# Performance work log

Measured on AMD Instinct MI355X. Metric: run time of the kernel, lower is better.

## Reference

```python
import jax, jax.numpy as jnp
import numpy as np

B, N, D = 4, 2048, 768
OUT = 768

def setup_inputs() -> dict:
    key = jax.random.key(0)
    k1, k2 = jax.random.split(key)
    x = jax.random.normal(k1, (B, N, D), dtype=jnp.float32)
    kernel = jax.random.normal(k2, (3, D, OUT), dtype=jnp.float32) * 0.02
    return {"x": x, "kernel": kernel}

def reference(x, kernel):
    # Single-head attention with shared QKV kernel stack [3, D, OUT]
    q = jnp.einsum('bnd,do->bno', x, kernel[0])
    k = jnp.einsum('bnd,do->bno', x, kernel[1])
    v = jnp.einsum('bnd,do->bno', x, kernel[2])
    # NOTE: original divides by 64**0.5 == 8 regardless of dims (faithful)
    scores = jnp.einsum('bqo,bko->bqk', q, k) / 8.0
    attn = jax.nn.softmax(scores, axis=-1)
    return jnp.einsum('bqk,bko->bqo', attn, v)
```

## Files before the change

### kernel.cpp

```cpp
#include <hip/hip_runtime.h>
#include <hip/hip_bf16.h>

constexpr int B_ = 4, N_ = 2048, D_ = 768, OUT_ = 768;
constexpr int M_ = B_ * N_;

typedef __attribute__((ext_vector_type(8))) short short8;
typedef __attribute__((ext_vector_type(4))) float floatx4;

__device__ __forceinline__ unsigned short f2bfu(float f) {
    union { __hip_bfloat16 b; unsigned short u; } cv;
    cv.b = __float2bfloat16(f);
    return cv.u;
}

#define GLOAD_LDS16(g, l)                                                     \
    __builtin_amdgcn_global_load_lds(                                         \
        (const __attribute__((address_space(1))) void*)(g),                   \
        (__attribute__((address_space(3))) void*)(l), 16, 0, 0)

template <int BM>
__device__ __forceinline__ void gemm_core(
    const __hip_bfloat16* __restrict__ a_base, int lda,
    const __hip_bfloat16* __restrict__ b_base, int ldb,
    int m0, int n0, int K,
    __hip_bfloat16* As, __hip_bfloat16* Bs,
    floatx4 (&acc)[BM / 32][4]) {
    constexpr int MF = BM / 32;
    const int tid  = threadIdx.x;
    const int wave = tid >> 6, lane = tid & 63;
    const int wm = (wave >> 1) * (BM / 2), wn = (wave & 1) * 64;
    const int lrow = lane & 15, kq = lane >> 4;
    const int sw = lrow & 7;

    for (int k0 = 0; k0 < K; k0 += 64) {
#pragma unroll
        for (int i = 0; i < MF; ++i) {
            const int u = i * 256 + tid;
            const int row = u >> 3, cg = (u & 7) ^ (row & 7);
            const __hip_bfloat16* g =
                a_base + (size_t)(m0 + row) * lda + k0 + cg * 8;
            GLOAD_LDS16(g, As + (size_t)(i * 256 + wave * 64) * 8);
        }
#pragma unroll
        for (int i = 0; i < 4; ++i) {
            const int u = i * 256 + tid;
            const int row = u >> 3, cg = (u & 7) ^ (row & 7);
            const __hip_bfloat16* g =
                b_base + (size_t)(n0 + row) * ldb + k0 + cg * 8;
            GLOAD_LDS16(g, Bs + (size_t)(i * 256 + wave * 64) * 8);
        }
        __syncthreads();

#pragma unroll
        for (int s = 0; s < 2; ++s) {
            short8 af[MF], bfr[4];
#pragma unroll
            for (int t = 0; t < MF; ++t) {
                const int row = wm + t * 16 + lrow;
                const int slot = (s * 4 + kq) ^ sw;
                af[t] = *(const short8*)(As + row * 64 + slot * 8);
            }
#pragma unroll
            for (int t = 0; t < 4; ++t) {
                const int row = wn + t * 16 + lrow;
                const int slot = (s * 4 + kq) ^ sw;
                bfr[t] = *(const short8*)(Bs + row * 64 + slot * 8);
            }
#pragma unroll
            for (int mi = 0; mi < MF; ++mi)
#pragma unroll
                for (int ni = 0; ni < 4; ++ni)
                    acc[mi][ni] = __builtin_amdgcn_mfma_f32_16x16x32_bf16(
                        af[mi], bfr[ni], acc[mi][ni], 0, 0, 0);
        }
        __syncthreads();
    }
}

__global__ __launch_bounds__(256)
void prep(const float* __restrict__ x, const float* __restrict__ w,
          __hip_bfloat16* __restrict__ xb, __hip_bfloat16* __restrict__ wt,
          float* __restrict__ l) {
    __shared__ float t[32][33];
    const int tid = threadIdx.x;
    if (blockIdx.x < 3072) {
        const size_t i = (size_t)blockIdx.x * 2048 + (size_t)tid * 8;
        float4 a = *(const float4*)(x + i);
        float4 b = *(const float4*)(x + i + 4);
        *(ushort4*)((unsigned short*)xb + i) =
            make_ushort4(f2bfu(a.x), f2bfu(a.y), f2bfu(a.z), f2bfu(a.w));
        *(ushort4*)((unsigned short*)xb + i + 4) =
            make_ushort4(f2bfu(b.x), f2bfu(b.y), f2bfu(b.z), f2bfu(b.w));
    } else if (blockIdx.x < 4800) {
        const int bid = blockIdx.x - 3072;
        const int s = bid / 576, rem = bid % 576;
        const int d0 = (rem / 24) * 32, o0 = (rem % 24) * 32;
        const int tx = tid & 31, ty = tid >> 5;
        const float* ws = w + (size_t)s * D_ * OUT_;
        __hip_bfloat16* wts = wt + (size_t)s * OUT_ * D_;
#pragma unroll
        for (int i = 0; i < 4; ++i)
            t[ty + 8 * i][tx] = ws[(size_t)(d0 + ty + 8 * i) * OUT_ + o0 + tx];
        __syncthreads();
#pragma unroll
        for (int i = 0; i < 4; ++i)
            wts[(size_t)(o0 + ty + 8 * i) * D_ + d0 + tx] =
                __float2bfloat16(t[tx][ty + 8 * i]);
    } else {
        float4* l4 = (float4*)l;
#pragma unroll
        for (int i = 0; i < 8; ++i) l4[i * 256 + tid] = make_float4(0, 0, 0, 0);
    }
}

__global__ __launch_bounds__(256)
void qkv_mfma(const __hip_bfloat16* __restrict__ xb,
              const __hip_bfloat16* __restrict__ wt,
              __hip_bfloat16* __restrict__ q, __hip_bfloat16* __restrict__ k,
              __hip_bfloat16* __restrict__ vt) {
    __shared__ __align__(16) char smem[34816];
    __hip_bfloat16* As = (__hip_bfloat16*)smem;
    __hip_bfloat16* Bs = As + 128 * 64;
    const int s = blockIdx.z;
    const int m0 = blockIdx.x * 128, n0 = blockIdx.y * 128;
    floatx4 acc[4][4] = {};
    gemm_core<128>(xb, D_, wt + (size_t)s * OUT_ * D_, D_, m0, n0, D_, As, Bs,
                   acc);

    const int tid = threadIdx.x, wave = tid >> 6, lane = tid & 63;
    const int wm = (wave >> 1) * 64, wn = (wave & 1) * 64;
    const int lrow = lane & 15, kq = lane >> 4;
    unsigned short* E = (unsigned short*)smem;

    if (s < 2) {
#pragma unroll
        for (int mi = 0; mi < 4; ++mi)
#pragma unroll
            for (int ni = 0; ni < 4; ++ni) {
                const int n = wn + ni * 16 + lrow;
#pragma unroll
                for (int r = 0; r < 4; ++r)
                    E[(wm + mi * 16 + kq * 4 + r) * 136 + n] =
                        f2bfu(acc[mi][ni][r]);
            }
    } else {
#pragma unroll
        for (int mi = 0; mi < 4; ++mi)
#pragma unroll
            for (int ni = 0; ni < 4; ++ni) {
                const int n = wn + ni * 16 + lrow;
#pragma unroll
                for (int r = 0; r < 4; ++r)
                    E[n * 136 + wm + mi * 16 + kq * 4 + r] =
                        f2bfu(acc[mi][ni][r]);
            }
    }
    __syncthreads();

    if (s < 2) {
        __hip_bfloat16* out = (s == 0) ? q : k;
#pragma unroll
        for (int i = 0; i < 8; ++i) {
            const int u = i * 256 + tid, row = u >> 4, c = u & 15;
            short8 v = *(const short8*)(E + row * 136 + c * 8);
            *(short8*)(out + (size_t)(m0 + row) * OUT_ + n0 + c * 8) = v;
        }
    } else {
        const int b = m0 >> 11, j0 = m0 & 2047;
#pragma unroll
        for (int i = 0; i < 8; ++i) {
            const int u = i * 256 + tid, nrow = u >> 4, c = u & 15;
            short8 v = *(const short8*)(E + nrow * 136 + c * 8);
            *(short8*)(vt + ((size_t)b * OUT_ + n0 + nrow) * N_ + j0 + c * 8) =
                v;
        }
    }
}

__global__ __launch_bounds__(256)
void scores_mfma(const __hip_bfloat16* __restrict__ q,
                 const __hip_bfloat16* __restrict__ k,
                 __hip_bfloat16* __restrict__ pt, float* __restrict__ l) {
    __shared__ __align__(16) char smem[34816];
    __hip_bfloat16* As = (__hip_bfloat16*)smem;
    __hip_bfloat16* Bs = As + 128 * 64;
    const int b = blockIdx.z;
    const int m0 = blockIdx.x * 128, n0 = blockIdx.y * 128;
    floatx4 acc[4][4] = {};
    gemm_core<128>(q + (size_t)b * N_ * OUT_, OUT_,
                   k + (size_t)b * N_ * OUT_, OUT_, m0, n0, OUT_, As, Bs, acc);

    const int tid = threadIdx.x, wave = tid >> 6, lane = tid & 63;
    const int wm = (wave >> 1) * 64, wn = (wave & 1) * 64;
    const int lrow = lane & 15, kq = lane >> 4;

    float rs[4][4];
#pragma unroll
    for (int mi = 0; mi < 4; ++mi)
#pragma unroll
        for (int r = 0; r < 4; ++r) rs[mi][r] = 0.0f;
#pragma unroll
    for (int mi = 0; mi < 4; ++mi)
#pragma unroll
        for (int ni = 0; ni < 4; ++ni)
#pragma unroll
            for (int r = 0; r < 4; ++r) {
                const float e = __expf(acc[mi][ni][r] * 0.125f - 8.0f);
                acc[mi][ni][r] = e;
                rs[mi][r] += e;
            }
#pragma unroll
    for (int mi = 0; mi < 4; ++mi)
#pragma unroll
        for (int r = 0; r < 4; ++r) {
            float v = rs[mi][r];
            v += __shfl_xor(v, 1, 64);
            v += __shfl_xor(v, 2, 64);
            v += __shfl_xor(v, 4, 64);
            v += __shfl_xor(v, 8, 64);
            if (lrow == 0)
                atomicAdd(&l[(size_t)b * N_ + m0 + wm + mi * 16 + kq * 4 + r],
                          v);
        }

    unsigned short* E = (unsigned short*)smem;
#pragma unroll
    for (int mi = 0; mi < 4; ++mi)
#pragma unroll
        for (int ni = 0; ni < 4; ++ni) {
            const int n = wn + ni * 16 + lrow;
#pragma unroll
            for (int r = 0; r < 4; ++r)
                E[(wm + mi * 16 + kq * 4 + r) * 136 + n] =
                    f2bfu(acc[mi][ni][r]);
        }
    __syncthreads();
    __hip_bfloat16* pb = pt + (size_t)b * N_ * N_;
#pragma unroll
    for (int i = 0; i < 8; ++i) {
        const int u = i * 256 + tid, row = u >> 4, c = u & 15;
        short8 v = *(const short8*)(E + row * 136 + c * 8);
        *(short8*)(pb + (size_t)(m0 + row) * N_ + n0 + c * 8) = v;
    }
}

__global__ __launch_bounds__(256)
void pv_mfma(const __hip_bfloat16* __restrict__ pt,
             const __hip_bfloat16* __restrict__ vt,
             const float* __restrict__ l, float* __restrict__ out) {
    __shared__ __align__(16) __hip_bfloat16 As[64 * 64];
    __shared__ __align__(16) __hip_bfloat16 Bs[128 * 64];
    const int b = blockIdx.z;
    const int m0 = blockIdx.x * 64, n0 = blockIdx.y * 128;
    floatx4 acc[2][4] = {};
    gemm_core<64>(pt + (size_t)b * N_ * N_, N_,
                  vt + (size_t)b * OUT_ * N_, N_, m0, n0, N_, As, Bs, acc);

    const int tid = threadIdx.x, wave = tid >> 6, lane = tid & 63;
    const int wm = (wave >> 1) * 32, wn = (wave & 1) * 64;
    const int lrow = lane & 15, kq = lane >> 4;
    const float* lb = l + (size_t)b * N_;
    float inv[2][4];
#pragma unroll
    for (int mi = 0; mi < 2; ++mi)
#pragma unroll
        for (int r = 0; r < 4; ++r)
            inv[mi][r] = 1.0f / lb[m0 + wm + mi * 16 + kq * 4 + r];
#pragma unroll
    for (int mi = 0; mi < 2; ++mi)
#pragma unroll
        for (int ni = 0; ni < 4; ++ni) {
            const int n = n0 + wn + ni * 16 + lrow;
#pragma unroll
            for (int r = 0; r < 4; ++r) {
                const int i = m0 + wm + mi * 16 + kq * 4 + r;
                out[((size_t)b * N_ + i) * OUT_ + n] =
                    acc[mi][ni][r] * inv[mi][r];
            }
        }
}

extern "C" void kernel_launch(void* const* d_in, const int* in_sizes, int n_in,
                              void* d_out, int out_size, void* d_ws, size_t ws_size,
                              hipStream_t stream) {
    const float* x = (const float*)d_in[0];
    const float* w = (const float*)d_in[1];
    float* out = (float*)d_out;

    __hip_bfloat16* q  = (__hip_bfloat16*)d_ws;
    __hip_bfloat16* k  = q + (size_t)M_ * OUT_;
    __hip_bfloat16* vt = k + (size_t)M_ * OUT_;
    __hip_bfloat16* xb = vt + (size_t)M_ * OUT_;
    __hip_bfloat16* wt = xb + (size_t)M_ * D_;
    float* l = (float*)(wt + (size_t)3 * OUT_ * D_);
    __hip_bfloat16* pt = (__hip_bfloat16*)(l + M_);

    prep<<<dim3(4801), dim3(256), 0, stream>>>(x, w, xb, wt, l);
    qkv_mfma<<<dim3(M_ / 128, OUT_ / 128, 3), dim3(256), 0, stream>>>(
        xb, wt, q, k, vt);
    scores_mfma<<<dim3(N_ / 128, N_ / 128, B_), dim3(256), 0, stream>>>(
        q, k, pt, l);
    pv_mfma<<<dim3(N_ / 64, OUT_ / 128, B_), dim3(256), 0, stream>>>(
        pt, vt, l, out);
}
```

Baseline: 202.2 us.

## Use 256x256 tiles with 4-stage async LDS pipeline and split-K PV

Replaces the 128x128 (and 64x128) GEMM core with a 512-thread 256x256 tile core that uses a 4-deep ring of direct global-to-LDS loads, explicit vmcnt waits and MFMA priority boosting. Epilogues for q, k and scores now store directly from registers without LDS staging. PV is split into two K halves that accumulate into a zero-initialized output with float atomics, which is why prep now also clears the output. The aim is more operand reuse per tile and overlap of loads with MFMA work. In exchange it uses 128 KB of LDS, makes fewer and larger blocks that may underfill the GPU, and adds atomic traffic.

After: 227.5 us. 1.13x slower.

```diff
diff --git a/kernel.cpp b/kernel.cpp
--- a/kernel.cpp
+++ b/kernel.cpp
@@ -18,69 +18,95 @@
         (const __attribute__((address_space(1))) void*)(g),                   \
         (__attribute__((address_space(3))) void*)(l), 16, 0, 0)
 
-template <int BM>
-__device__ __forceinline__ void gemm_core(
-    const __hip_bfloat16* __restrict__ a_base, int lda,
-    const __hip_bfloat16* __restrict__ b_base, int ldb,
-    int m0, int n0, int K,
-    __hip_bfloat16* As, __hip_bfloat16* Bs,
-    floatx4 (&acc)[BM / 32][4]) {
-    constexpr int MF = BM / 32;
-    const int tid  = threadIdx.x;
+template <int NT>
+__device__ __forceinline__ void gemm256_core(
+    const __hip_bfloat16* __restrict__ aG, int lda,
+    const __hip_bfloat16* __restrict__ bG, int ldb,
+    unsigned short* LDS, floatx4 (&acc)[8][4]) {
+    const int tid = threadIdx.x;
     const int wave = tid >> 6, lane = tid & 63;
-    const int wm = (wave >> 1) * (BM / 2), wn = (wave & 1) * 64;
     const int lrow = lane & 15, kq = lane >> 4;
-    const int sw = lrow & 7;
-
-    for (int k0 = 0; k0 < K; k0 += 64) {
-#pragma unroll
-        for (int i = 0; i < MF; ++i) {
-            const int u = i * 256 + tid;
-            const int row = u >> 3, cg = (u & 7) ^ (row & 7);
-            const __hip_bfloat16* g =
-                a_base + (size_t)(m0 + row) * lda + k0 + cg * 8;
-            GLOAD_LDS16(g, As + (size_t)(i * 256 + wave * 64) * 8);
-        }
-#pragma unroll
-        for (int i = 0; i < 4; ++i) {
-            const int u = i * 256 + tid;
-            const int row = u >> 3, cg = (u & 7) ^ (row & 7);
-            const __hip_bfloat16* g =
-                b_base + (size_t)(n0 + row) * ldb + k0 + cg * 8;
-            GLOAD_LDS16(g, Bs + (size_t)(i * 256 + wave * 64) * 8);
-        }
-        __syncthreads();
-
-#pragma unroll
-        for (int s = 0; s < 2; ++s) {
-            short8 af[MF], bfr[4];
-#pragma unroll
-            for (int t = 0; t < MF; ++t) {
-                const int row = wm + t * 16 + lrow;
-                const int slot = (s * 4 + kq) ^ sw;
-                af[t] = *(const short8*)(As + row * 64 + slot * 8);
-            }
-#pragma unroll
-            for (int t = 0; t < 4; ++t) {
-                const int row = wn + t * 16 + lrow;
-                const int slot = (s * 4 + kq) ^ sw;
-                bfr[t] = *(const short8*)(Bs + row * 64 + slot * 8);
-            }
-#pragma unroll
-            for (int mi = 0; mi < MF; ++mi)
-#pragma unroll
-                for (int ni = 0; ni < 4; ++ni)
-                    acc[mi][ni] = __builtin_amdgcn_mfma_f32_16x16x32_bf16(
-                        af[mi], bfr[ni], acc[mi][ni], 0, 0, 0);
-        }
-        __syncthreads();
-    }
+    const int wm = (wave >> 2) * 128, wn = (wave & 3) * 64;
+
+    const __hip_bfloat16* sA[2];
+    const __hip_bfloat16* sB[2];
+#pragma unroll
+    for (int i = 0; i < 2; ++i) {
+        const int u = i * 512 + tid;
+        const int p = u >> 3, g = (u & 7) ^ (p & 7);
+        const int row = 2 * p + (g >> 2), ch = g & 3;
+        sA[i] = aG + (size_t)row * lda + ch * 8;
+        sB[i] = bG + (size_t)row * ldb + ch * 8;
+    }
+    int offA[8], offB[4];
+#pragma unroll
+    for (int mi = 0; mi < 8; ++mi) {
+        const int row = wm + mi * 16 + lrow;
+        const int p = row >> 1, g = ((row & 1) << 2) | kq;
+        offA[mi] = p * 64 + ((g ^ (p & 7)) * 8);
+    }
+#pragma unroll
+    for (int ni = 0; ni < 4; ++ni) {
+        const int row = wn + ni * 16 + lrow;
+        const int p = row >> 1, g = ((row & 1) << 2) | kq;
+        offB[ni] = p * 64 + ((g ^ (p & 7)) * 8);
+    }
+
+#define STAGE_T(ti)                                                        \
+    do {                                                                   \
+        unsigned short* dst_ = LDS + ((ti) & 3) * 16384 + wave * 512;      \
+        GLOAD_LDS16(sA[0], dst_);                                          \
+        GLOAD_LDS16(sA[1], dst_ + 4096);                                   \
+        GLOAD_LDS16(sB[0], dst_ + 8192);                                   \
+        GLOAD_LDS16(sB[1], dst_ + 12288);                                  \
+        sA[0] += 32; sA[1] += 32; sB[0] += 32; sB[1] += 32;                \
+    } while (0)
+
+    STAGE_T(0);
+    STAGE_T(1);
+    STAGE_T(2);
+    asm volatile("s_waitcnt vmcnt(8)" ::: "memory");
+    __builtin_amdgcn_s_barrier();
+    __builtin_amdgcn_sched_barrier(0);
+
+    for (int t = 0; t < NT; ++t) {
+        if (t + 3 < NT) STAGE_T(t + 3);
+        const unsigned short* Sa = LDS + (t & 3) * 16384;
+        const unsigned short* Sb = Sa + 8192;
+        short8 bf[4], af[8];
+#pragma unroll
+        for (int ni = 0; ni < 4; ++ni)
+            bf[ni] = *(const short8*)(Sb + offB[ni]);
+#pragma unroll
+        for (int mi = 0; mi < 8; ++mi)
+            af[mi] = *(const short8*)(Sa + offA[mi]);
+        __builtin_amdgcn_s_setprio(1);
+#pragma unroll
+        for (int mi = 0; mi < 8; ++mi)
+#pragma unroll
+            for (int ni = 0; ni < 4; ++ni)
+                acc[mi][ni] = __builtin_amdgcn_mfma_f32_16x16x32_bf16(
+                    af[mi], bf[ni], acc[mi][ni], 0, 0, 0);
+        __builtin_amdgcn_s_setprio(0);
+        if (t + 3 < NT) {
+            asm volatile("s_waitcnt vmcnt(8)" ::: "memory");
+        } else if (t + 2 < NT) {
+            asm volatile("s_waitcnt vmcnt(4)" ::: "memory");
+        } else if (t + 1 < NT) {
+            asm volatile("s_waitcnt vmcnt(0)" ::: "memory");
+        }
+        if (t + 1 < NT) {
+            __builtin_amdgcn_s_barrier();
+            __builtin_amdgcn_sched_barrier(0);
+        }
+    }
+#undef STAGE_T
 }
 
 __global__ __launch_bounds__(256)
 void prep(const float* __restrict__ x, const float* __restrict__ w,
           __hip_bfloat16* __restrict__ xb, __hip_bfloat16* __restrict__ wt,
-          float* __restrict__ l) {
+          float* __restrict__ l, float* __restrict__ out) {
     __shared__ float t[32][33];
     const int tid = threadIdx.x;
     if (blockIdx.x < 3072) {
@@ -106,101 +132,97 @@
         for (int i = 0; i < 4; ++i)
             wts[(size_t)(o0 + ty + 8 * i) * D_ + d0 + tx] =
                 __float2bfloat16(t[tx][ty + 8 * i]);
+    } else if (blockIdx.x == 4800) {
+        float4* l4 = (float4*)l;
+#pragma unroll
+        for (int i = 0; i < 8; ++i) l4[i * 256 + tid] = make_float4(0, 0, 0, 0);
     } else {
-        float4* l4 = (float4*)l;
-#pragma unroll
-        for (int i = 0; i < 8; ++i) l4[i * 256 + tid] = make_float4(0, 0, 0, 0);
-    }
-}
-
-__global__ __launch_bounds__(256)
+        const size_t bid2 = blockIdx.x - 4801;
+        ((float4*)out)[bid2 * 256 + tid] = make_float4(0, 0, 0, 0);
+    }
+}
+
+__global__ __launch_bounds__(512, 2)
 void qkv_mfma(const __hip_bfloat16* __restrict__ xb,
               const __hip_bfloat16* __restrict__ wt,
               __hip_bfloat16* __restrict__ q, __hip_bfloat16* __restrict__ k,
               __hip_bfloat16* __restrict__ vt) {
-    __shared__ __align__(16) char smem[34816];
-    __hip_bfloat16* As = (__hip_bfloat16*)smem;
-    __hip_bfloat16* Bs = As + 128 * 64;
+    __shared__ __align__(16) unsigned short LDS[65536];
     const int s = blockIdx.z;
-    const int m0 = blockIdx.x * 128, n0 = blockIdx.y * 128;
-    floatx4 acc[4][4] = {};
-    gemm_core<128>(xb, D_, wt + (size_t)s * OUT_ * D_, D_, m0, n0, D_, As, Bs,
-                   acc);
+    const int m0 = blockIdx.x * 256, n0 = blockIdx.y * 256;
+    floatx4 acc[8][4] = {};
+    gemm256_core<24>(xb + (size_t)m0 * D_, D_,
+                     wt + (size_t)s * OUT_ * D_ + (size_t)n0 * D_, D_, LDS,
+                     acc);
 
     const int tid = threadIdx.x, wave = tid >> 6, lane = tid & 63;
-    const int wm = (wave >> 1) * 64, wn = (wave & 1) * 64;
     const int lrow = lane & 15, kq = lane >> 4;
-    unsigned short* E = (unsigned short*)smem;
+    const int wm = (wave >> 2) * 128, wn = (wave & 3) * 64;
 
     if (s < 2) {
-#pragma unroll
-        for (int mi = 0; mi < 4; ++mi)
-#pragma unroll
-            for (int ni = 0; ni < 4; ++ni) {
-                const int n = wn + ni * 16 + lrow;
-#pragma unroll
-                for (int r = 0; r < 4; ++r)
-                    E[(wm + mi * 16 + kq * 4 + r) * 136 + n] =
-                        f2bfu(acc[mi][ni][r]);
+        unsigned short* outp = (unsigned short*)(s == 0 ? q : k);
+#pragma unroll
+        for (int mi = 0; mi < 8; ++mi)
+#pragma unroll
+            for (int r = 0; r < 4; ++r) {
+                const size_t ro =
+                    (size_t)(m0 + wm + mi * 16 + kq * 4 + r) * OUT_ + n0 + wn;
+#pragma unroll
+                for (int ni = 0; ni < 4; ++ni)
+                    outp[ro + ni * 16 + lrow] = f2bfu(acc[mi][ni][r]);
             }
     } else {
-#pragma unroll
-        for (int mi = 0; mi < 4; ++mi)
-#pragma unroll
-            for (int ni = 0; ni < 4; ++ni) {
-                const int n = wn + ni * 16 + lrow;
-#pragma unroll
-                for (int r = 0; r < 4; ++r)
-                    E[n * 136 + wm + mi * 16 + kq * 4 + r] =
-                        f2bfu(acc[mi][ni][r]);
+        unsigned short* E = LDS;
+        const int b = m0 >> 11, j0 = m0 & 2047;
+#pragma unroll
+        for (int h = 0; h < 2; ++h) {
+            __syncthreads();
+            if ((wave >> 2) == h) {
+#pragma unroll
+                for (int ni = 0; ni < 4; ++ni)
+#pragma unroll
+                    for (int mi = 0; mi < 8; ++mi)
+#pragma unroll
+                        for (int r = 0; r < 4; ++r)
+                            E[(wn + ni * 16 + lrow) * 136 + mi * 16 + kq * 4 +
+                              r] = f2bfu(acc[mi][ni][r]);
             }
-    }
-    __syncthreads();
-
-    if (s < 2) {
-        __hip_bfloat16* out = (s == 0) ? q : k;
-#pragma unroll
-        for (int i = 0; i < 8; ++i) {
-            const int u = i * 256 + tid, row = u >> 4, c = u & 15;
-            short8 v = *(const short8*)(E + row * 136 + c * 8);
-            *(short8*)(out + (size_t)(m0 + row) * OUT_ + n0 + c * 8) = v;
-        }
-    } else {
-        const int b = m0 >> 11, j0 = m0 & 2047;
-#pragma unroll
-        for (int i = 0; i < 8; ++i) {
-            const int u = i * 256 + tid, nrow = u >> 4, c = u & 15;
-            short8 v = *(const short8*)(E + nrow * 136 + c * 8);
-            *(short8*)(vt + ((size_t)b * OUT_ + n0 + nrow) * N_ + j0 + c * 8) =
-                v;
-        }
-    }
-}
-
-__global__ __launch_bounds__(256)
+            __syncthreads();
+#pragma unroll
+            for (int i = 0; i < 8; ++i) {
+                const int u = i * 512 + tid, nr = u >> 4, c = u & 15;
+                short8 vv = *(const short8*)(E + nr * 136 + c * 8);
+                *(short8*)((unsigned short*)vt +
+                           ((size_t)b * OUT_ + n0 + nr) * N_ + j0 + h * 128 +
+                           c * 8) = vv;
+            }
+        }
+    }
+}
+
+__global__ __launch_bounds__(512, 2)
 void scores_mfma(const __hip_bfloat16* __restrict__ q,
                  const __hip_bfloat16* __restrict__ k,
                  __hip_bfloat16* __restrict__ pt, float* __restrict__ l) {
-    __shared__ __align__(16) char smem[34816];
-    __hip_bfloat16* As = (__hip_bfloat16*)smem;
-    __hip_bfloat16* Bs = As + 128 * 64;
+    __shared__ __align__(16) unsigned short LDS[65536];
     const int b = blockIdx.z;
-    const int m0 = blockIdx.x * 128, n0 = blockIdx.y * 128;
-    floatx4 acc[4][4] = {};
-    gemm_core<128>(q + (size_t)b * N_ * OUT_, OUT_,
-                   k + (size_t)b * N_ * OUT_, OUT_, m0, n0, OUT_, As, Bs, acc);
+    const int m0 = blockIdx.x * 256, n0 = blockIdx.y * 256;
+    floatx4 acc[8][4] = {};
+    gemm256_core<24>(q + (size_t)b * N_ * OUT_ + (size_t)m0 * OUT_, OUT_,
+                     k + (size_t)b * N_ * OUT_ + (size_t)n0 * OUT_, OUT_, LDS,
+                     acc);
 
     const int tid = threadIdx.x, wave = tid >> 6, lane = tid & 63;
-    const int wm = (wave >> 1) * 64, wn = (wave & 1) * 64;
     const int lrow = lane & 15, kq = lane >> 4;
-
-    float rs[4][4];
-#pragma unroll
-    for (int mi = 0; mi < 4; ++mi)
+    const int wm = (wave >> 2) * 128, wn = (wave & 3) * 64;
+
+    float rs[8][4];
+#pragma unroll
+    for (int mi = 0; mi < 8; ++mi)
 #pragma unroll
         for (int r = 0; r < 4; ++r) rs[mi][r] = 0.0f;
 #pragma unroll
-    for (int mi = 0; mi < 4; ++mi)
+    for (int mi = 0; mi < 8; ++mi)
 #pragma unroll
         for (int ni = 0; ni < 4; ++ni)
 #pragma unroll
@@ -210,7 +232,7 @@
                 rs[mi][r] += e;
             }
 #pragma unroll
-    for (int mi = 0; mi < 4; ++mi)
+    for (int mi = 0; mi < 8; ++mi)
 #pragma unroll
         for (int r = 0; r < 4; ++r) {
             float v = rs[mi][r];
@@ -222,67 +244,53 @@
                 atomicAdd(&l[(size_t)b * N_ + m0 + wm + mi * 16 + kq * 4 + r],
                           v);
         }
-
-    unsigned short* E = (unsigned short*)smem;
-#pragma unroll
-    for (int mi = 0; mi < 4; ++mi)
-#pragma unroll
-        for (int ni = 0; ni < 4; ++ni) {
-            const int n = wn + ni * 16 + lrow;
-#pragma unroll
-            for (int r = 0; r < 4; ++r)
-                E[(wm + mi * 16 + kq * 4 + r) * 136 + n] =
-                    f2bfu(acc[mi][ni][r]);
-        }
-    __syncthreads();
-    __hip_bfloat16* pb = pt + (size_t)b * N_ * N_;
-#pragma unroll
-    for (int i = 0; i < 8; ++i) {
-        const int u = i * 256 + tid, row = u >> 4, c = u & 15;
-        short8 v = *(const short8*)(E + row * 136 + c * 8);
-        *(short8*)(pb + (size_t)(m0 + row) * N_ + n0 + c * 8) = v;
-    }
-}
-
-__global__ __launch_bounds__(256)
+    unsigned short* pb = (unsigned short*)pt + (size_t)b * N_ * N_;
+#pragma unroll
+    for (int mi = 0; mi < 8; ++mi)
+#pragma unroll
+        for (int r = 0; r < 4; ++r) {
+            const size_t ro =
+                (size_t)(m0 + wm + mi * 16 + kq * 4 + r) * N_ + n0 + wn;
+#pragma unroll
+            for (int ni = 0; ni < 4; ++ni)
+                pb[ro + ni * 16 + lrow] = f2bfu(acc[mi][ni][r]);
+        }
+}
+
+__global__ __launch_bounds__(512, 2)
 void pv_mfma(const __hip_bfloat16* __restrict__ pt,
              const __hip_bfloat16* __restrict__ vt,
              const float* __restrict__ l, float* __restrict__ out) {
-    __shared__ __align__(16) __hip_bfloat16 As[64 * 64];
-    __shared__ __align__(16) __hip_bfloat16 Bs[128 * 64];
-    const int b = blockIdx.z;
-    const int m0 = blockIdx.x * 64, n0 = blockIdx.y * 128;
-    floatx4 acc[2][4] = {};
-    gemm_core<64>(pt + (size_t)b * N_ * N_, N_,
-                  vt + (size_t)b * OUT_ * N_, N_, m0, n0, N_, As, Bs, acc);
+    __shared__ __align__(16) unsigned short LDS[65536];
+    const int b = blockIdx.z >> 1, h = blockIdx.z & 1;
+    const int m0 = blockIdx.x * 256, n0 = blockIdx.y * 256;
+    floatx4 acc[8][4] = {};
+    gemm256_core<32>(
+        pt + (size_t)b * N_ * N_ + (size_t)m0 * N_ + h * 1024, N_,
+        vt + (size_t)b * OUT_ * N_ + (size_t)n0 * N_ + h * 1024, N_, LDS, acc);
 
     const int tid = threadIdx.x, wave = tid >> 6, lane = tid & 63;
-    const int wm = (wave >> 1) * 32, wn = (wave & 1) * 64;
     const int lrow = lane & 15, kq = lane >> 4;
-    const float* lb = l + (size_t)b * N_;
-    float inv[2][4];
-#pragma unroll
-    for (int mi = 0; mi < 2; ++mi)
-#pragma unroll
-        for (int r = 0; r < 4; ++r)
-            inv[mi][r] = 1.0f / lb[m0 + wm + mi * 16 + kq * 4 + r];
-#pragma unroll
-    for (int mi = 0; mi < 2; ++mi)
-#pragma unroll
-        for (int ni = 0; ni < 4; ++ni) {
-            const int n = n0 + wn + ni * 16 + lrow;
-#pragma unroll
-            for (int r = 0; r < 4; ++r) {
-                const int i = m0 + wm + mi * 16 + kq * 4 + r;
-                out[((size_t)b * N_ + i) * OUT_ + n] =
-                    acc[mi][ni][r] * inv[mi][r];
-            }
+    const int wm = (wave >> 2) * 128, wn = (wave & 3) * 64;
+    const float* lb = l + (size_t)b * N_ + m0 + wm;
+#pragma unroll
+    for (int mi = 0; mi < 8; ++mi)
+#pragma unroll
+        for (int r = 0; r < 4; ++r) {
+            const float inv = 1.0f / lb[mi * 16 + kq * 4 + r];
+            float* o = out +
+                       ((size_t)b * N_ + m0 + wm + mi * 16 + kq * 4 + r) *
+                           OUT_ +
+                       n0 + wn;
+#pragma unroll
+            for (int ni = 0; ni < 4; ++ni)
+                atomicAdd(o + ni * 16 + lrow, acc[mi][ni][r] * inv);
         }
 }
 
 extern "C" void kernel_launch(void* const* d_in, const int* in_sizes, int n_in,
-                              void* d_out, int out_size, void* d_ws, size_t ws_size,
-                              hipStream_t stream) {
+                              void* d_out, int out_size, void* d_ws,
+                              size_t ws_size, hipStream_t stream) {
     const float* x = (const float*)d_in[0];
     const float* w = (const float*)d_in[1];
     float* out = (float*)d_out;
@@ -295,11 +303,8 @@
     float* l = (float*)(wt + (size_t)3 * OUT_ * D_);
     __hip_bfloat16* pt = (__hip_bfloat16*)(l + M_);
 
-    prep<<<dim3(4801), dim3(256), 0, stream>>>(x, w, xb, wt, l);
-    qkv_mfma<<<dim3(M_ / 128, OUT_ / 128, 3), dim3(256), 0, stream>>>(
-        xb, wt, q, k, vt);
-    scores_mfma<<<dim3(N_ / 128, N_ / 128, B_), dim3(256), 0, stream>>>(
-        q, k, pt, l);
-    pv_mfma<<<dim3(N_ / 64, OUT_ / 128, B_), dim3(256), 0, stream>>>(
-        pt, vt, l, out);
-}
+    prep<<<dim3(10945), dim3(256), 0, stream>>>(x, w, xb, wt, l, out);
+    qkv_mfma<<<dim3(32, 3, 3), dim3(512), 0, stream>>>(xb, wt, q, k, vt);
+    scores_mfma<<<dim3(8, 8, 4), dim3(512), 0, stream>>>(q, k, pt, l);
+    pv_mfma<<<dim3(8, 3, 8), dim3(512), 0, stream>>>(pt, vt, l, out);
+}
```

## Triple-buffer GEMM mainloop with async LDS loads and larger 512-thread tiles

Applied to the files above, without the earlier changes.

Replaces the single-buffered K-loop GEMM core with a three-stage ring buffer fed by direct global-to-LDS loads. It issues the loads two K-steps ahead and synchronises with explicit vmcnt waits and one barrier per step, so memory traffic overlaps MFMA work. The K step drops from 64 to 32, and the LDS layout pairs rows with an XOR swizzle. Blocks grow to 512 threads with larger output tiles (128x256 for QKV and scores, 128x128 for PV), trading fewer blocks and lower occupancy for more operand reuse. The epilogues are adjusted to the new tile shapes, and the PV output store is reordered per row.

New measurement: 189.7 us. 1.07x faster.

```diff
diff --git a/kernel.cpp b/kernel.cpp
--- a/kernel.cpp
+++ b/kernel.cpp
@@ -18,62 +18,89 @@
         (const __attribute__((address_space(1))) void*)(g),                   \
         (__attribute__((address_space(3))) void*)(l), 16, 0, 0)
 
-template <int BM>
-__device__ __forceinline__ void gemm_core(
-    const __hip_bfloat16* __restrict__ a_base, int lda,
-    const __hip_bfloat16* __restrict__ b_base, int ldb,
-    int m0, int n0, int K,
-    __hip_bfloat16* As, __hip_bfloat16* Bs,
-    floatx4 (&acc)[BM / 32][4]) {
-    constexpr int MF = BM / 32;
-    const int tid  = threadIdx.x;
+#define MFMA_BF16 __builtin_amdgcn_mfma_f32_16x16x32_bf16
+#define SBAR __builtin_amdgcn_s_barrier
+#define SCHED0 __builtin_amdgcn_sched_barrier
+
+template <int MFR, int NT>
+__device__ __forceinline__ void gemm_tb(
+    const __hip_bfloat16* __restrict__ aG, int lda,
+    const __hip_bfloat16* __restrict__ bG, int ldb,
+    unsigned short* LDS, floatx4 (&acc)[MFR][4]) {
+    constexpr int BSLOT = (MFR == 4) ? 8192 : 4096;
+    constexpr int BUFS = 4096 + BSLOT;
+    constexpr int LOADS = (MFR == 4) ? 3 : 2;
+    const int tid = threadIdx.x;
     const int wave = tid >> 6, lane = tid & 63;
-    const int wm = (wave >> 1) * (BM / 2), wn = (wave & 1) * 64;
-    const int lrow = lane & 15, kq = lane >> 4;
-    const int sw = lrow & 7;
-
-    for (int k0 = 0; k0 < K; k0 += 64) {
-#pragma unroll
-        for (int i = 0; i < MF; ++i) {
-            const int u = i * 256 + tid;
-            const int row = u >> 3, cg = (u & 7) ^ (row & 7);
-            const __hip_bfloat16* g =
-                a_base + (size_t)(m0 + row) * lda + k0 + cg * 8;
-            GLOAD_LDS16(g, As + (size_t)(i * 256 + wave * 64) * 8);
-        }
-#pragma unroll
-        for (int i = 0; i < 4; ++i) {
-            const int u = i * 256 + tid;
-            const int row = u >> 3, cg = (u & 7) ^ (row & 7);
-            const __hip_bfloat16* g =
-                b_base + (size_t)(n0 + row) * ldb + k0 + cg * 8;
-            GLOAD_LDS16(g, Bs + (size_t)(i * 256 + wave * 64) * 8);
-        }
-        __syncthreads();
-
-#pragma unroll
-        for (int s = 0; s < 2; ++s) {
-            short8 af[MF], bfr[4];
-#pragma unroll
-            for (int t = 0; t < MF; ++t) {
-                const int row = wm + t * 16 + lrow;
-                const int slot = (s * 4 + kq) ^ sw;
-                af[t] = *(const short8*)(As + row * 64 + slot * 8);
-            }
-#pragma unroll
-            for (int t = 0; t < 4; ++t) {
-                const int row = wn + t * 16 + lrow;
-                const int slot = (s * 4 + kq) ^ sw;
-                bfr[t] = *(const short8*)(Bs + row * 64 + slot * 8);
-            }
-#pragma unroll
-            for (int mi = 0; mi < MF; ++mi)
-#pragma unroll
-                for (int ni = 0; ni < 4; ++ni)
-                    acc[mi][ni] = __builtin_amdgcn_mfma_f32_16x16x32_bf16(
-                        af[mi], bfr[ni], acc[mi][ni], 0, 0, 0);
-        }
-        __syncthreads();
+    const int lr = lane & 15, kq = lane >> 4;
+    const int wm = (MFR == 4) ? (wave >> 2) * 64 : (wave >> 1) * 32;
+    const int wn = (MFR == 4) ? (wave & 3) * 64 : (wave & 1) * 64;
+
+    const int p0 = tid >> 3, g0 = (tid & 7) ^ (p0 & 7);
+    const __hip_bfloat16* pa =
+        aG + (size_t)(2 * p0 + (g0 >> 2)) * lda + (g0 & 3) * 8;
+    const __hip_bfloat16* pb0 =
+        bG + (size_t)(2 * p0 + (g0 >> 2)) * ldb + (g0 & 3) * 8;
+    const __hip_bfloat16* pb1 = bG;
+    if constexpr (MFR == 4) {
+        const int u = 512 + tid, p1 = u >> 3, g1 = (u & 7) ^ (p1 & 7);
+        pb1 = bG + (size_t)(2 * p1 + (g1 >> 2)) * ldb + (g1 & 3) * 8;
+    }
+
+    int oa[MFR], ob[4];
+#pragma unroll
+    for (int mi = 0; mi < MFR; ++mi) {
+        const int r = wm + mi * 16 + lr, p = r >> 1;
+        const int g = ((r & 1) << 2) | kq;
+        oa[mi] = p * 64 + ((g ^ (p & 7)) * 8);
+    }
+#pragma unroll
+    for (int ni = 0; ni < 4; ++ni) {
+        const int r = wn + ni * 16 + lr, p = r >> 1;
+        const int g = ((r & 1) << 2) | kq;
+        ob[ni] = p * 64 + ((g ^ (p & 7)) * 8);
+    }
+
+    auto STAGE = [&](int tt, int buf) {
+        unsigned short* d = LDS + buf * BUFS + wave * 512;
+        GLOAD_LDS16(pa + tt * 32, d);
+        GLOAD_LDS16(pb0 + tt * 32, d + 4096);
+        if constexpr (MFR == 4) GLOAD_LDS16(pb1 + tt * 32, d + 8192);
+    };
+
+    STAGE(0, 0);
+    STAGE(1, 1);
+    asm volatile("s_waitcnt vmcnt(%0)" ::"i"(LOADS) : "memory");
+    SBAR();
+    SCHED0(0);
+
+    int bR = 0, bS = 2;
+    for (int t = 0; t < NT; ++t) {
+        const unsigned short* Ab = LDS + bR * BUFS;
+        const unsigned short* Bb = Ab + 4096;
+        short8 af[MFR], bf[4];
+#pragma unroll
+        for (int mi = 0; mi < MFR; ++mi)
+            af[mi] = *(const short8*)(Ab + oa[mi]);
+#pragma unroll
+        for (int ni = 0; ni < 4; ++ni)
+            bf[ni] = *(const short8*)(Bb + ob[ni]);
+        if (t + 2 < NT) STAGE(t + 2, bS);
+#pragma unroll
+        for (int mi = 0; mi < MFR; ++mi)
+#pragma unroll
+            for (int ni = 0; ni < 4; ++ni)
+                acc[mi][ni] = MFMA_BF16(af[mi], bf[ni], acc[mi][ni], 0, 0, 0);
+        if (t + 2 < NT)
+            asm volatile("s_waitcnt vmcnt(%0)" ::"i"(LOADS) : "memory");
+        else if (t + 1 < NT)
+            asm volatile("s_waitcnt vmcnt(0)" ::: "memory");
+        if (t + 1 < NT) {
+            SBAR();
+            SCHED0(0);
+        }
+        bR = (bR == 2) ? 0 : bR + 1;
+        bS = (bS == 2) ? 0 : bS + 1;
     }
 }
 
@@ -113,26 +140,25 @@
     }
 }
 
-__global__ __launch_bounds__(256)
+__global__ __launch_bounds__(512, 4)
 void qkv_mfma(const __hip_bfloat16* __restrict__ xb,
               const __hip_bfloat16* __restrict__ wt,
               __hip_bfloat16* __restrict__ q, __hip_bfloat16* __restrict__ k,
               __hip_bfloat16* __restrict__ vt) {
-    __shared__ __align__(16) char smem[34816];
-    __hip_bfloat16* As = (__hip_bfloat16*)smem;
-    __hip_bfloat16* Bs = As + 128 * 64;
+    __shared__ __align__(16) unsigned short LDS[36864];
     const int s = blockIdx.z;
-    const int m0 = blockIdx.x * 128, n0 = blockIdx.y * 128;
+    const int m0 = blockIdx.x * 128, n0 = blockIdx.y * 256;
     floatx4 acc[4][4] = {};
-    gemm_core<128>(xb, D_, wt + (size_t)s * OUT_ * D_, D_, m0, n0, D_, As, Bs,
-                   acc);
+    gemm_tb<4, 24>(xb + (size_t)m0 * D_, D_,
+                   wt + (size_t)s * OUT_ * D_ + (size_t)n0 * D_, D_, LDS, acc);
 
     const int tid = threadIdx.x, wave = tid >> 6, lane = tid & 63;
-    const int wm = (wave >> 1) * 64, wn = (wave & 1) * 64;
     const int lrow = lane & 15, kq = lane >> 4;
-    unsigned short* E = (unsigned short*)smem;
+    const int wm = (wave >> 2) * 64, wn = (wave & 3) * 64;
+    unsigned short* E = LDS;
 
     if (s < 2) {
+        __syncthreads();
 #pragma unroll
         for (int mi = 0; mi < 4; ++mi)
 #pragma unroll
@@ -140,10 +166,19 @@
                 const int n = wn + ni * 16 + lrow;
 #pragma unroll
                 for (int r = 0; r < 4; ++r)
-                    E[(wm + mi * 16 + kq * 4 + r) * 136 + n] =
+                    E[(wm + mi * 16 + kq * 4 + r) * 264 + n] =
                         f2bfu(acc[mi][ni][r]);
             }
+        __syncthreads();
+        unsigned short* outp = (unsigned short*)(s == 0 ? q : k);
+#pragma unroll
+        for (int i = 0; i < 8; ++i) {
+            const int u = i * 512 + tid, row = u >> 5, c = u & 31;
+            *(short8*)(outp + (size_t)(m0 + row) * OUT_ + n0 + c * 8) =
+                *(const short8*)(E + row * 264 + c * 8);
+        }
     } else {
+        __syncthreads();
 #pragma unroll
         for (int mi = 0; mi < 4; ++mi)
 #pragma unroll
@@ -154,45 +189,32 @@
                     E[n * 136 + wm + mi * 16 + kq * 4 + r] =
                         f2bfu(acc[mi][ni][r]);
             }
-    }
-    __syncthreads();
-
-    if (s < 2) {
-        __hip_bfloat16* out = (s == 0) ? q : k;
+        __syncthreads();
+        const int b = m0 >> 11, j0 = m0 & 2047;
 #pragma unroll
         for (int i = 0; i < 8; ++i) {
-            const int u = i * 256 + tid, row = u >> 4, c = u & 15;
-            short8 v = *(const short8*)(E + row * 136 + c * 8);
-            *(short8*)(out + (size_t)(m0 + row) * OUT_ + n0 + c * 8) = v;
-        }
-    } else {
-        const int b = m0 >> 11, j0 = m0 & 2047;
-#pragma unroll
-        for (int i = 0; i < 8; ++i) {
-            const int u = i * 256 + tid, nrow = u >> 4, c = u & 15;
-            short8 v = *(const short8*)(E + nrow * 136 + c * 8);
-            *(short8*)(vt + ((size_t)b * OUT_ + n0 + nrow) * N_ + j0 + c * 8) =
-                v;
-        }
-    }
-}
-
-__global__ __launch_bounds__(256)
+            const int u = i * 512 + tid, nr = u >> 4, c = u & 15;
+            *(short8*)((unsigned short*)vt + ((size_t)b * OUT_ + n0 + nr) * N_ +
+                       j0 + c * 8) = *(const short8*)(E + nr * 136 + c * 8);
+        }
+    }
+}
+
+__global__ __launch_bounds__(512, 4)
 void scores_mfma(const __hip_bfloat16* __restrict__ q,
                  const __hip_bfloat16* __restrict__ k,
                  __hip_bfloat16* __restrict__ pt, float* __restrict__ l) {
-    __shared__ __align__(16) char smem[34816];
-    __hip_bfloat16* As = (__hip_bfloat16*)smem;
-    __hip_bfloat16* Bs = As + 128 * 64;
+    __shared__ __align__(16) unsigned short LDS[36864];
     const int b = blockIdx.z;
-    const int m0 = blockIdx.x * 128, n0 = blockIdx.y * 128;
+    const int m0 = blockIdx.x * 128, n0 = blockIdx.y * 256;
     floatx4 acc[4][4] = {};
-    gemm_core<128>(q + (size_t)b * N_ * OUT_, OUT_,
-                   k + (size_t)b * N_ * OUT_, OUT_, m0, n0, OUT_, As, Bs, acc);
+    gemm_tb<4, 24>(q + (size_t)b * N_ * OUT_ + (size_t)m0 * OUT_, OUT_,
+                   k + (size_t)b * N_ * OUT_ + (size_t)n0 * OUT_, OUT_, LDS,
+                   acc);
 
     const int tid = threadIdx.x, wave = tid >> 6, lane = tid & 63;
-    const int wm = (wave >> 1) * 64, wn = (wave & 1) * 64;
     const int lrow = lane & 15, kq = lane >> 4;
+    const int wm = (wave >> 2) * 64, wn = (wave & 3) * 64;
 
     float rs[4][4];
 #pragma unroll
@@ -223,7 +245,9 @@
                           v);
         }
 
-    unsigned short* E = (unsigned short*)smem;
+    unsigned short* E = LDS;
+    unsigned short* pb = (unsigned short*)pt + (size_t)b * N_ * N_;
+    __syncthreads();
 #pragma unroll
     for (int mi = 0; mi < 4; ++mi)
 #pragma unroll
@@ -231,58 +255,51 @@
             const int n = wn + ni * 16 + lrow;
 #pragma unroll
             for (int r = 0; r < 4; ++r)
-                E[(wm + mi * 16 + kq * 4 + r) * 136 + n] =
+                E[(wm + mi * 16 + kq * 4 + r) * 258 + n] =
                     f2bfu(acc[mi][ni][r]);
         }
     __syncthreads();
-    __hip_bfloat16* pb = pt + (size_t)b * N_ * N_;
 #pragma unroll
     for (int i = 0; i < 8; ++i) {
-        const int u = i * 256 + tid, row = u >> 4, c = u & 15;
-        short8 v = *(const short8*)(E + row * 136 + c * 8);
-        *(short8*)(pb + (size_t)(m0 + row) * N_ + n0 + c * 8) = v;
-    }
-}
-
-__global__ __launch_bounds__(256)
+        const int u = i * 512 + tid, row = u >> 5, c = u & 31;
+        *(short8*)(pb + (size_t)(m0 + row) * N_ + n0 + c * 8) =
+            *(const short8*)(E + row * 258 + c * 8);
+    }
+}
+
+__global__ __launch_bounds__(512, 4)
 void pv_mfma(const __hip_bfloat16* __restrict__ pt,
              const __hip_bfloat16* __restrict__ vt,
              const float* __restrict__ l, float* __restrict__ out) {
-    __shared__ __align__(16) __hip_bfloat16 As[64 * 64];
-    __shared__ __align__(16) __hip_bfloat16 Bs[128 * 64];
+    __shared__ __align__(16) unsigned short LDS[24576];
     const int b = blockIdx.z;
-    const int m0 = blockIdx.x * 64, n0 = blockIdx.y * 128;
+    const int m0 = blockIdx.x * 128, n0 = blockIdx.y * 128;
     floatx4 acc[2][4] = {};
-    gemm_core<64>(pt + (size_t)b * N_ * N_, N_,
-                  vt + (size_t)b * OUT_ * N_, N_, m0, n0, N_, As, Bs, acc);
+    gemm_tb<2, 64>(pt + (size_t)b * N_ * N_ + (size_t)m0 * N_, N_,
+                   vt + (size_t)b * OUT_ * N_ + (size_t)n0 * N_, N_, LDS, acc);
 
     const int tid = threadIdx.x, wave = tid >> 6, lane = tid & 63;
+    const int lrow = lane & 15, kq = lane >> 4;
     const int wm = (wave >> 1) * 32, wn = (wave & 1) * 64;
-    const int lrow = lane & 15, kq = lane >> 4;
-    const float* lb = l + (size_t)b * N_;
-    float inv[2][4];
+    const float* lb = l + (size_t)b * N_ + m0 + wm;
 #pragma unroll
     for (int mi = 0; mi < 2; ++mi)
 #pragma unroll
-        for (int r = 0; r < 4; ++r)
-            inv[mi][r] = 1.0f / lb[m0 + wm + mi * 16 + kq * 4 + r];
-#pragma unroll
-    for (int mi = 0; mi < 2; ++mi)
-#pragma unroll
-        for (int ni = 0; ni < 4; ++ni) {
-            const int n = n0 + wn + ni * 16 + lrow;
-#pragma unroll
-            for (int r = 0; r < 4; ++r) {
-                const int i = m0 + wm + mi * 16 + kq * 4 + r;
-                out[((size_t)b * N_ + i) * OUT_ + n] =
-                    acc[mi][ni][r] * inv[mi][r];
-            }
+        for (int r = 0; r < 4; ++r) {
+            const float inv = 1.0f / lb[mi * 16 + kq * 4 + r];
+            float* o = out +
+                       ((size_t)b * N_ + m0 + wm + mi * 16 + kq * 4 + r) *
+                           OUT_ +
+                       n0 + wn;
+#pragma unroll
+            for (int ni = 0; ni < 4; ++ni)
+                o[ni * 16 + lrow] = acc[mi][ni][r] * inv;
         }
 }
 
 extern "C" void kernel_launch(void* const* d_in, const int* in_sizes, int n_in,
-                              void* d_out, int out_size, void* d_ws, size_t ws_size,
-                              hipStream_t stream) {
+                              void* d_out, int out_size, void* d_ws,
+                              size_t ws_size, hipStream_t stream) {
     const float* x = (const float*)d_in[0];
     const float* w = (const float*)d_in[1];
     float* out = (float*)d_out;
@@ -296,10 +313,7 @@
     __hip_bfloat16* pt = (__hip_bfloat16*)(l + M_);
 
     prep<<<dim3(4801), dim3(256), 0, stream>>>(x, w, xb, wt, l);
-    qkv_mfma<<<dim3(M_ / 128, OUT_ / 128, 3), dim3(256), 0, stream>>>(
-        xb, wt, q, k, vt);
-    scores_mfma<<<dim3(N_ / 128, N_ / 128, B_), dim3(256), 0, stream>>>(
-        q, k, pt, l);
-    pv_mfma<<<dim3(N_ / 64, OUT_ / 128, B_), dim3(256), 0, stream>>>(
-        pt, vt, l, out);
-}
+    qkv_mfma<<<dim3(64, 3, 3), dim3(512), 0, stream>>>(xb, wt, q, k, vt);
+    scores_mfma<<<dim3(16, 8, 4), dim3(512), 0, stream>>>(q, k, pt, l);
+    pv_mfma<<<dim3(16, 6, 4), dim3(512), 0, stream>>>(pt, vt, l, out);
+}
```
